# Performance work log

Hardware: AMD Instinct MI355X
Metric: run time of the kernel (lower is better)

## Reference

```python
import jax, jax.numpy as jnp
import numpy as np

N_NODES = 50000
N_EDGES = 1600000
D_IN = 256
N_HEADS = 4
D_OUT = 32
NEG_SLOPE = 0.2


def setup_inputs() -> dict:
    key = jax.random.key(0)
    ks = jax.random.split(key, 7)
    return {
        "feat": jax.random.normal(ks[0], (N_NODES, D_IN), dtype=jnp.float32),
        "fc_w": jax.random.normal(ks[1], (N_HEADS * D_OUT, D_IN), dtype=jnp.float32) * 0.05,
        "attn_l": jax.random.normal(ks[2], (1, N_HEADS, D_OUT), dtype=jnp.float32) * 0.1,
        "attn_r": jax.random.normal(ks[3], (1, N_HEADS, D_OUT), dtype=jnp.float32) * 0.1,
        "bias": jax.random.normal(ks[4], (N_HEADS * D_OUT,), dtype=jnp.float32) * 0.01,
        "src": jax.random.randint(ks[5], (N_EDGES,), 0, N_NODES, dtype=jnp.int32),
        "dst": jax.random.randint(ks[6], (N_EDGES,), 0, N_NODES, dtype=jnp.int32),
    }


def reference(feat, fc_w, attn_l, attn_r, bias, src, dst):
    N = feat.shape[0]
    H, D = attn_l.shape[1], attn_l.shape[2]
    # projected features: [N, H, D] (torch Linear: x @ W.T)
    h = (feat @ fc_w.T).reshape(N, H, D)
    # per-node attention logits: [N, H]
    el = (h * attn_l).sum(-1)
    er = (h * attn_r).sum(-1)
    # per-edge score with leaky relu: [E, H]
    e = el[src] + er[dst]
    e = jnp.where(e > 0, e, NEG_SLOPE * e)
    # edge softmax normalized over incoming edges of each dst node
    m = jax.ops.segment_max(e, dst, num_segments=N)
    m = jnp.where(jnp.isfinite(m), m, 0.0)  # nodes with no in-edges
    ex = jnp.exp(e - m[dst])
    denom = jax.ops.segment_sum(ex, dst, num_segments=N)
    a = ex / jnp.maximum(denom[dst], 1e-9)  # [E, H]
    # weighted scatter-aggregate: [N, H, D]
    msg = h[src] * a[:, :, None]
    out = jax.ops.segment_sum(msg, dst, num_segments=N)
    out = out + bias.reshape(1, H, D)
    return out
```

## Files before the change

### kernel.cpp

```cpp
#include <hip/hip_runtime.h>
#include <hip/hip_bf16.h>
#include <math.h>

#define D_IN   256
#define HD     128
#define NHEAD  4
#define NEG_SLOPE 0.2f
#define MAXB  1024
#define BCAP  2560

typedef _Float16 h8 __attribute__((ext_vector_type(8)));
typedef _Float16 h4 __attribute__((ext_vector_type(4)));
typedef _Float16 h2 __attribute__((ext_vector_type(2)));
typedef float f4 __attribute__((ext_vector_type(4)));

#define SWZ(row, byte) ((byte) ^ (((row) & 7) << 4))

__global__ __launch_bounds__(256) void fused_k(
        const float* __restrict__ feat, const float* __restrict__ fcw,
        const float* __restrict__ attn_l, const float* __restrict__ attn_r,
        unsigned int* __restrict__ hbuf, float* __restrict__ el, float* __restrict__ er,
        const int* __restrict__ src, const int* __restrict__ dst,
        int* __restrict__ gcur, unsigned int* __restrict__ pairs,
        int N, int E, int B, int GB) {
    __shared__ __align__(16) unsigned char smem[64 * 512];
    const int t = threadIdx.x;

    if ((int)blockIdx.x >= GB) {
        int* lcnt  = (int*)smem;
        int* lbase = lcnt + MAXB;
        for (int i = t; i < B; i += 256) lcnt[i] = 0;
        __syncthreads();
        const int base = ((int)blockIdx.x - GB) * 4096;
        int sv[16], dv[16];
        #pragma unroll
        for (int k = 0; k < 16; ++k) {
            int idx = base + k * 256 + t;
            if (idx < E) {
                sv[k] = src[idx];
                dv[k] = dst[idx];
                atomicAdd(&lcnt[dv[k] >> 6], 1);
            } else dv[k] = -1;
        }
        __syncthreads();
        for (int i = t; i < B; i += 256) {
            int c = lcnt[i];
            lbase[i] = c ? atomicAdd(&gcur[i], c) : 0;
            lcnt[i] = 0;
        }
        __syncthreads();
        #pragma unroll
        for (int k = 0; k < 16; ++k) {
            if (dv[k] >= 0) {
                int b = dv[k] >> 6;
                int r = lbase[b] + atomicAdd(&lcnt[b], 1);
                if (r < BCAP)
                    pairs[(size_t)b * BCAP + r] = ((unsigned int)sv[k] << 6) | (unsigned int)(dv[k] & 63);
            }
        }
        return;
    }

    unsigned char* lds_raw = smem;
    const int l  = t & 63;
    const int w  = t >> 6;
    const int l4 = l >> 4;
    const int lm = l & 15;
    const int n0 = blockIdx.x * 64;

    h8 breg[2][8];
    #pragma unroll
    for (int jt = 0; jt < 2; ++jt) {
        const float* wrow = fcw + (size_t)(w * 32 + jt * 16 + lm) * D_IN;
        #pragma unroll
        for (int ks = 0; ks < 8; ++ks) {
            int k = ks * 32 + l4 * 8;
            float4 a = *(const float4*)&wrow[k];
            float4 b = *(const float4*)&wrow[k + 4];
            h8 p = {(_Float16)a.x, (_Float16)a.y, (_Float16)a.z, (_Float16)a.w,
                    (_Float16)b.x, (_Float16)b.y, (_Float16)b.z, (_Float16)b.w};
            breg[jt][ks] = p;
        }
    }

    #pragma unroll
    for (int i = 0; i < 16; ++i) {
        int idx = t + 256 * i;
        int row = idx >> 6, c4 = idx & 63;
        float4 v = make_float4(0.f, 0.f, 0.f, 0.f);
        if (n0 + row < N) v = *(const float4*)&feat[(size_t)(n0 + row) * D_IN + c4 * 4];
        h4 p = {(_Float16)v.x, (_Float16)v.y, (_Float16)v.z, (_Float16)v.w};
        *(h4*)(lds_raw + row * 512 + SWZ(row, c4 * 8)) = p;
    }
    __syncthreads();

    f4 acc[4][2] = {};
    #pragma unroll
    for (int ks = 0; ks < 8; ++ks) {
        #pragma unroll
        for (int mt = 0; mt < 4; ++mt) {
            int row = mt * 16 + lm;
            h8 af = *(const h8*)(lds_raw + row * 512 + SWZ(row, (ks * 32 + l4 * 8) * 2));
            acc[mt][0] = __builtin_amdgcn_mfma_f32_16x16x32_f16(af, breg[0][ks], acc[mt][0], 0, 0, 0);
            acc[mt][1] = __builtin_amdgcn_mfma_f32_16x16x32_f16(af, breg[1][ks], acc[mt][1], 0, 0, 0);
        }
    }

    float al[2], ar[2];
    #pragma unroll
    for (int jt = 0; jt < 2; ++jt) {
        al[jt] = attn_l[w * 32 + jt * 16 + lm];
        ar[jt] = attn_r[w * 32 + jt * 16 + lm];
    }
    #pragma unroll
    for (int mt = 0; mt < 4; ++mt) {
        #pragma unroll
        for (int r = 0; r < 4; ++r) {
            float vl = acc[mt][0][r] * al[0] + acc[mt][1][r] * al[1];
            float vr = acc[mt][0][r] * ar[0] + acc[mt][1][r] * ar[1];
            #pragma unroll
            for (int o = 1; o < 16; o <<= 1) {
                vl += __shfl_xor(vl, o);
                vr += __shfl_xor(vr, o);
            }
            int node = n0 + mt * 16 + l4 * 4 + r;
            if (lm == 0 && node < N) {
                el[node * NHEAD + w] = vl;
                er[node * NHEAD + w] = vr;
            }
        }
    }

    __syncthreads();
    unsigned short* hl = (unsigned short*)lds_raw;
    #pragma unroll
    for (int mt = 0; mt < 4; ++mt)
        #pragma unroll
        for (int jt = 0; jt < 2; ++jt)
            #pragma unroll
            for (int r = 0; r < 4; ++r) {
                int node_local = mt * 16 + l4 * 4 + r;
                int ch = w * 32 + jt * 16 + lm;
                _Float16 hf = (_Float16)acc[mt][jt][r];
                hl[node_local * 128 + ch] = __builtin_bit_cast(unsigned short, hf);
            }
    __syncthreads();
    const unsigned int* hu = (const unsigned int*)lds_raw;
    #pragma unroll
    for (int i = 0; i < 16; ++i) {
        int idx = t + 256 * i;
        int row = idx >> 6, c = idx & 63;
        if (n0 + row < N) hbuf[(size_t)(n0 + row) * 64 + c] = hu[row * 64 + c];
    }
}

__global__ __launch_bounds__(256) void bucket_k(const unsigned int* __restrict__ pairs,
                                                const int* __restrict__ gcur,
                                                int* __restrict__ row_start,
                                                int* __restrict__ degs,
                                                int* __restrict__ srcs, int N) {
    __shared__ int cnt64[64];
    __shared__ int base64[64];
    const int b = blockIdx.x;
    const int t = threadIdx.x;
    const int lo = b * BCAP;
    const int len = min(gcur[b], BCAP);
    if (t < 64) cnt64[t] = 0;
    __syncthreads();
    for (int i = t; i < len; i += 256)
        atomicAdd(&cnt64[pairs[lo + i] & 63], 1);
    __syncthreads();
    if (t < 64) {
        int v = cnt64[t];
        int x = v;
        #pragma unroll
        for (int o = 1; o < 64; o <<= 1) {
            int y = __shfl_up(x, o);
            if (t >= o) x += y;
        }
        int excl = lo + x - v;
        base64[t] = excl;
        int d = b * 64 + t;
        if (d < N) { row_start[d] = excl; degs[d] = v; }
        cnt64[t] = 0;
    }
    __syncthreads();
    for (int i = lo + t; i < lo + len; i += 256) {
        unsigned int p = pairs[i];
        int ld = p & 63;
        int r = atomicAdd(&cnt64[ld], 1);
        srcs[base64[ld] + r] = (int)(p >> 6);
    }
}

__global__ __launch_bounds__(256) void agg_k(
        const int* __restrict__ row_start, const int* __restrict__ degs,
        const int* __restrict__ srcs,
        const float* __restrict__ el, const float* __restrict__ er,
        const unsigned int* __restrict__ hbuf, const float* __restrict__ bias,
        float* __restrict__ out, int N) {
    const int l = threadIdx.x & 63;
    const int d = blockIdx.x * 4 + (threadIdx.x >> 6);
    if (d >= N) return;
    const int q  = l >> 4;
    const int es = l & 15;
    const int hc = es >> 2;
    const int base = row_start[d];
    const int deg  = degs[d];
    const float erd = er[d * NHEAD + q];

    float acc[8] = {0.f, 0.f, 0.f, 0.f, 0.f, 0.f, 0.f, 0.f};
    float den = 0.f;

    for (int c0 = 0; c0 < deg; c0 += 32) {
        const int clen = min(32, deg - c0);
        int s0 = 0, s1 = 0;
        float ex0 = 0.f, ex1 = 0.f;
        if (es < clen) {
            s0 = srcs[base + c0 + es];
            float v = el[s0 * NHEAD + q] + erd;
            v = v > 0.f ? v : NEG_SLOPE * v;
            ex0 = __expf(v);
            den += ex0;
        }
        if (es + 16 < clen) {
            s1 = srcs[base + c0 + es + 16];
            float v = el[s1 * NHEAD + q] + erd;
            v = v > 0.f ? v : NEG_SLOPE * v;
            ex1 = __expf(v);
            den += ex1;
        }
        for (int jj = 0; jj < clen; jj += 16) {
            uint4 hv[4];
            float exv[4];
            #pragma unroll
            for (int k = 0; k < 4; ++k) {
                int e4 = jj + k * 4 + q;
                int ls = e4 & 15;
                int sa = __shfl(s0, ls);
                int sb = __shfl(s1, ls);
                float ea = __shfl(ex0, hc * 16 + ls);
                float eb = __shfl(ex1, hc * 16 + ls);
                int s = (e4 < 16) ? sa : sb;
                exv[k] = (e4 < clen) ? ((e4 < 16) ? ea : eb) : 0.f;
                hv[k] = *(const uint4*)&hbuf[(size_t)s * 64 + es * 4];
            }
            #pragma unroll
            for (int k = 0; k < 4; ++k) {
                #pragma unroll
                for (int c = 0; c < 4; ++c) {
                    unsigned int u = (&hv[k].x)[c];
                    h2 p = __builtin_bit_cast(h2, u);
                    acc[2 * c]     += (float)p[0] * exv[k];
                    acc[2 * c + 1] += (float)p[1] * exv[k];
                }
            }
        }
    }

    #pragma unroll
    for (int c = 0; c < 8; ++c) {
        acc[c] += __shfl_xor(acc[c], 16);
        acc[c] += __shfl_xor(acc[c], 32);
    }
    #pragma unroll
    for (int o = 1; o < 16; o <<= 1) den += __shfl_xor(den, o);
    float denc = __shfl(den, hc << 4);

    if (q == 0) {
        float r = 1.0f / fmaxf(denc, 1e-9f);
        float4 b0 = *(const float4*)&bias[es * 8];
        float4 b1 = *(const float4*)&bias[es * 8 + 4];
        float4 o0 = make_float4(acc[0] * r + b0.x, acc[1] * r + b0.y,
                                acc[2] * r + b0.z, acc[3] * r + b0.w);
        float4 o1 = make_float4(acc[4] * r + b1.x, acc[5] * r + b1.y,
                                acc[6] * r + b1.z, acc[7] * r + b1.w);
        *(float4*)&out[(size_t)d * HD + es * 8]     = o0;
        *(float4*)&out[(size_t)d * HD + es * 8 + 4] = o1;
    }
}

extern "C" void kernel_launch(void* const* d_in, const int* in_sizes, int n_in,
                              void* d_out, int out_size, void* d_ws, size_t ws_size,
                              hipStream_t stream) {
    const float* feat   = (const float*)d_in[0];
    const float* fcw    = (const float*)d_in[1];
    const float* attn_l = (const float*)d_in[2];
    const float* attn_r = (const float*)d_in[3];
    const float* bias   = (const float*)d_in[4];
    const int*   src    = (const int*)d_in[5];
    const int*   dst    = (const int*)d_in[6];
    float* out = (float*)d_out;

    const int N = in_sizes[0] / D_IN;
    const int E = in_sizes[5];
    const int B = (N + 63) >> 6;

    unsigned int* hbuf = (unsigned int*)d_ws;
    float* el        = (float*)(hbuf + (size_t)N * 64);
    float* er        = el + (size_t)N * NHEAD;
    unsigned int* pairs = (unsigned int*)(er + (size_t)N * NHEAD);
    int*   srcs      = (int*)(pairs + (size_t)B * BCAP);
    int*   row_start = srcs + (size_t)B * BCAP;
    int*   degs      = row_start + N;
    int*   gcur      = degs + N;

    const int GB  = (N + 63) / 64;
    const int ebl = (E + 4095) / 4096;

    hipMemsetAsync(gcur, 0, (size_t)B * sizeof(int), stream);
    fused_k<<<GB + ebl, 256, 0, stream>>>(feat, fcw, attn_l, attn_r, hbuf, el, er,
                                          src, dst, gcur, pairs, N, E, B, GB);
    bucket_k<<<B, 256, 0, stream>>>(pairs, gcur, row_start, degs, srcs, N);
    agg_k<<<(N + 3) / 4, 256, 0, stream>>>(row_start, degs, srcs, el, er, hbuf, bias, out, N);
}
```

Measured before the change: 131.7 us.

## Tile edges by source range and aggregate multiple destinations per wave for L2 locality

Edges are bucketed by destination block and by source-node quarter (src>>14), so bucketing produces per-(dst-block, src-tile) segments. The aggregation kernel has each wave own up to nine destination nodes and sweep the source tiles in order. The goal is to keep the gathered hbuf rows within a smaller working set that fits in cache. The aggregation also drops the shuffle-based 4-edge interleave in favour of one 32-bit channel pair per lane with four edges unrolled, which removes cross-lane reductions. In exchange it adds more segments and a smaller per-segment capacity (edges beyond it are dropped), fewer waves in flight, and possible load imbalance across waves.

```diff
diff --git a/kernel.cpp b/kernel.cpp
--- a/kernel.cpp
+++ b/kernel.cpp
@@ -6,8 +6,10 @@
 #define HD     128
 #define NHEAD  4
 #define NEG_SLOPE 0.2f
-#define MAXB  1024
-#define BCAP  2560
+#define T      4
+#define MAXK   4096
+#define SEGCAP 1024
+#define KMAX   9
 
 typedef _Float16 h8 __attribute__((ext_vector_type(8)));
 typedef _Float16 h4 __attribute__((ext_vector_type(4)));
@@ -22,14 +24,14 @@
         unsigned int* __restrict__ hbuf, float* __restrict__ el, float* __restrict__ er,
         const int* __restrict__ src, const int* __restrict__ dst,
         int* __restrict__ gcur, unsigned int* __restrict__ pairs,
-        int N, int E, int B, int GB) {
+        int N, int E, int B4, int GB) {
     __shared__ __align__(16) unsigned char smem[64 * 512];
     const int t = threadIdx.x;
 
     if ((int)blockIdx.x >= GB) {
         int* lcnt  = (int*)smem;
-        int* lbase = lcnt + MAXB;
-        for (int i = t; i < B; i += 256) lcnt[i] = 0;
+        int* lbase = lcnt + MAXK;
+        for (int i = t; i < B4; i += 256) lcnt[i] = 0;
         __syncthreads();
         const int base = ((int)blockIdx.x - GB) * 4096;
         int sv[16], dv[16];
@@ -39,11 +41,11 @@
             if (idx < E) {
                 sv[k] = src[idx];
                 dv[k] = dst[idx];
-                atomicAdd(&lcnt[dv[k] >> 6], 1);
+                atomicAdd(&lcnt[(dv[k] >> 6) * T + (sv[k] >> 14)], 1);
             } else dv[k] = -1;
         }
         __syncthreads();
-        for (int i = t; i < B; i += 256) {
+        for (int i = t; i < B4; i += 256) {
             int c = lcnt[i];
             lbase[i] = c ? atomicAdd(&gcur[i], c) : 0;
             lcnt[i] = 0;
@@ -52,10 +54,11 @@
         #pragma unroll
         for (int k = 0; k < 16; ++k) {
             if (dv[k] >= 0) {
-                int b = dv[k] >> 6;
-                int r = lbase[b] + atomicAdd(&lcnt[b], 1);
-                if (r < BCAP)
-                    pairs[(size_t)b * BCAP + r] = ((unsigned int)sv[k] << 6) | (unsigned int)(dv[k] & 63);
+                int key = (dv[k] >> 6) * T + (sv[k] >> 14);
+                int r = lbase[key] + atomicAdd(&lcnt[key], 1);
+                if (r < SEGCAP)
+                    pairs[(size_t)key * SEGCAP + r] =
+                        ((unsigned int)sv[k] << 6) | (unsigned int)(dv[k] & 63);
             }
         }
         return;
@@ -156,15 +159,16 @@
 
 __global__ __launch_bounds__(256) void bucket_k(const unsigned int* __restrict__ pairs,
                                                 const int* __restrict__ gcur,
-                                                int* __restrict__ row_start,
-                                                int* __restrict__ degs,
+                                                int2* __restrict__ rs2,
                                                 int* __restrict__ srcs, int N) {
     __shared__ int cnt64[64];
     __shared__ int base64[64];
-    const int b = blockIdx.x;
+    const int key = blockIdx.x;
+    const int b   = key / T;
+    const int tl  = key - b * T;
     const int t = threadIdx.x;
-    const int lo = b * BCAP;
-    const int len = min(gcur[b], BCAP);
+    const int lo = key * SEGCAP;
+    const int len = min(gcur[key], SEGCAP);
     if (t < 64) cnt64[t] = 0;
     __syncthreads();
     for (int i = t; i < len; i += 256)
@@ -181,7 +185,7 @@
         int excl = lo + x - v;
         base64[t] = excl;
         int d = b * 64 + t;
-        if (d < N) { row_start[d] = excl; degs[d] = v; }
+        if (d < N) rs2[d * T + tl] = make_int2(excl, v);
         cnt64[t] = 0;
     }
     __syncthreads();
@@ -194,89 +198,74 @@
 }
 
 __global__ __launch_bounds__(256) void agg_k(
-        const int* __restrict__ row_start, const int* __restrict__ degs,
-        const int* __restrict__ srcs,
+        const int2* __restrict__ rs2, const int* __restrict__ srcs,
         const float* __restrict__ el, const float* __restrict__ er,
         const unsigned int* __restrict__ hbuf, const float* __restrict__ bias,
-        float* __restrict__ out, int N) {
-    const int l = threadIdx.x & 63;
-    const int d = blockIdx.x * 4 + (threadIdx.x >> 6);
-    if (d >= N) return;
-    const int q  = l >> 4;
-    const int es = l & 15;
-    const int hc = es >> 2;
-    const int base = row_start[d];
-    const int deg  = degs[d];
-    const float erd = er[d * NHEAD + q];
-
-    float acc[8] = {0.f, 0.f, 0.f, 0.f, 0.f, 0.f, 0.f, 0.f};
-    float den = 0.f;
-
-    for (int c0 = 0; c0 < deg; c0 += 32) {
-        const int clen = min(32, deg - c0);
-        int s0 = 0, s1 = 0;
-        float ex0 = 0.f, ex1 = 0.f;
-        if (es < clen) {
-            s0 = srcs[base + c0 + es];
-            float v = el[s0 * NHEAD + q] + erd;
-            v = v > 0.f ? v : NEG_SLOPE * v;
-            ex0 = __expf(v);
-            den += ex0;
-        }
-        if (es + 16 < clen) {
-            s1 = srcs[base + c0 + es + 16];
-            float v = el[s1 * NHEAD + q] + erd;
-            v = v > 0.f ? v : NEG_SLOPE * v;
-            ex1 = __expf(v);
-            den += ex1;
-        }
-        for (int jj = 0; jj < clen; jj += 16) {
-            uint4 hv[4];
-            float exv[4];
-            #pragma unroll
-            for (int k = 0; k < 4; ++k) {
-                int e4 = jj + k * 4 + q;
-                int ls = e4 & 15;
-                int sa = __shfl(s0, ls);
-                int sb = __shfl(s1, ls);
-                float ea = __shfl(ex0, hc * 16 + ls);
-                float eb = __shfl(ex1, hc * 16 + ls);
-                int s = (e4 < 16) ? sa : sb;
-                exv[k] = (e4 < clen) ? ((e4 < 16) ? ea : eb) : 0.f;
-                hv[k] = *(const uint4*)&hbuf[(size_t)s * 64 + es * 4];
-            }
-            #pragma unroll
-            for (int k = 0; k < 4; ++k) {
-                #pragma unroll
-                for (int c = 0; c < 4; ++c) {
-                    unsigned int u = (&hv[k].x)[c];
-                    h2 p = __builtin_bit_cast(h2, u);
-                    acc[2 * c]     += (float)p[0] * exv[k];
-                    acc[2 * c + 1] += (float)p[1] * exv[k];
+        float* __restrict__ out, int N, int stride) {
+    const int l  = threadIdx.x & 63;
+    const int g  = blockIdx.x * 4 + (threadIdx.x >> 6);
+    const int h  = l >> 4;
+
+    float ax[KMAX], ay[KMAX], dn[KMAX];
+    #pragma unroll
+    for (int k = 0; k < KMAX; ++k) { ax[k] = 0.f; ay[k] = 0.f; dn[k] = 0.f; }
+
+    for (int tl = 0; tl < T; ++tl) {
+        #pragma unroll
+        for (int k = 0; k < KMAX; ++k) {
+            const int d = g + k * stride;
+            if (d < N) {
+                const int2 bd = rs2[d * T + tl];
+                const int deg = bd.y;
+                if (deg > 0) {
+                    const float erd = er[d * NHEAD + h];
+                    for (int j = 0; j < deg; j += 4) {
+                        const int n = deg - j;
+                        const int jb = bd.x + j;
+                        int s0 = srcs[jb];
+                        int s1 = (n > 1) ? srcs[jb + 1] : 0;
+                        int s2 = (n > 2) ? srcs[jb + 2] : 0;
+                        int s3 = (n > 3) ? srcs[jb + 3] : 0;
+                        float e0 = el[s0 * NHEAD + h];
+                        float e1 = el[s1 * NHEAD + h];
+                        float e2 = el[s2 * NHEAD + h];
+                        float e3 = el[s3 * NHEAD + h];
+                        unsigned int v0 = hbuf[(size_t)s0 * 64 + l];
+                        unsigned int v1 = hbuf[(size_t)s1 * 64 + l];
+                        unsigned int v2 = hbuf[(size_t)s2 * 64 + l];
+                        unsigned int v3 = hbuf[(size_t)s3 * 64 + l];
+                        float q0 = e0 + erd; q0 = q0 > 0.f ? q0 : NEG_SLOPE * q0;
+                        float q1 = e1 + erd; q1 = q1 > 0.f ? q1 : NEG_SLOPE * q1;
+                        float q2 = e2 + erd; q2 = q2 > 0.f ? q2 : NEG_SLOPE * q2;
+                        float q3 = e3 + erd; q3 = q3 > 0.f ? q3 : NEG_SLOPE * q3;
+                        float x0 = __expf(q0);
+                        float x1 = (n > 1) ? __expf(q1) : 0.f;
+                        float x2 = (n > 2) ? __expf(q2) : 0.f;
+                        float x3 = (n > 3) ? __expf(q3) : 0.f;
+                        dn[k] += (x0 + x1) + (x2 + x3);
+                        h2 p0 = __builtin_bit_cast(h2, v0);
+                        h2 p1 = __builtin_bit_cast(h2, v1);
+                        h2 p2 = __builtin_bit_cast(h2, v2);
+                        h2 p3 = __builtin_bit_cast(h2, v3);
+                        ax[k] += (float)p0[0] * x0 + (float)p1[0] * x1
+                               + (float)p2[0] * x2 + (float)p3[0] * x3;
+                        ay[k] += (float)p0[1] * x0 + (float)p1[1] * x1
+                               + (float)p2[1] * x2 + (float)p3[1] * x3;
+                    }
                 }
             }
         }
     }
 
-    #pragma unroll
-    for (int c = 0; c < 8; ++c) {
-        acc[c] += __shfl_xor(acc[c], 16);
-        acc[c] += __shfl_xor(acc[c], 32);
-    }
-    #pragma unroll
-    for (int o = 1; o < 16; o <<= 1) den += __shfl_xor(den, o);
-    float denc = __shfl(den, hc << 4);
-
-    if (q == 0) {
-        float r = 1.0f / fmaxf(denc, 1e-9f);
-        float4 b0 = *(const float4*)&bias[es * 8];
-        float4 b1 = *(const float4*)&bias[es * 8 + 4];
-        float4 o0 = make_float4(acc[0] * r + b0.x, acc[1] * r + b0.y,
-                                acc[2] * r + b0.z, acc[3] * r + b0.w);
-        float4 o1 = make_float4(acc[4] * r + b1.x, acc[5] * r + b1.y,
-                                acc[6] * r + b1.z, acc[7] * r + b1.w);
-        *(float4*)&out[(size_t)d * HD + es * 8]     = o0;
-        *(float4*)&out[(size_t)d * HD + es * 8 + 4] = o1;
+    const float2 bb = *(const float2*)&bias[2 * l];
+    #pragma unroll
+    for (int k = 0; k < KMAX; ++k) {
+        const int d = g + k * stride;
+        if (d < N) {
+            float r = 1.0f / fmaxf(dn[k], 1e-9f);
+            float2 o2 = make_float2(ax[k] * r + bb.x, ay[k] * r + bb.y);
+            *(float2*)&out[(size_t)d * HD + 2 * l] = o2;
+        }
     }
 }
 
@@ -295,22 +284,25 @@
     const int N = in_sizes[0] / D_IN;
     const int E = in_sizes[5];
     const int B = (N + 63) >> 6;
+    const int B4 = B * T;
 
     unsigned int* hbuf = (unsigned int*)d_ws;
     float* el        = (float*)(hbuf + (size_t)N * 64);
     float* er        = el + (size_t)N * NHEAD;
     unsigned int* pairs = (unsigned int*)(er + (size_t)N * NHEAD);
-    int*   srcs      = (int*)(pairs + (size_t)B * BCAP);
-    int*   row_start = srcs + (size_t)B * BCAP;
-    int*   degs      = row_start + N;
-    int*   gcur      = degs + N;
+    int*   srcs      = (int*)(pairs + (size_t)B4 * SEGCAP);
+    int2*  rs2       = (int2*)(srcs + (size_t)B4 * SEGCAP);
+    int*   gcur      = (int*)(rs2 + (size_t)N * T);
 
     const int GB  = (N + 63) / 64;
     const int ebl = (E + 4095) / 4096;
 
-    hipMemsetAsync(gcur, 0, (size_t)B * sizeof(int), stream);
+    const int aggBlocks = (N + 4 * KMAX - 1) / (4 * KMAX);
+    const int stride = aggBlocks * 4;
+
+    hipMemsetAsync(gcur, 0, (size_t)B4 * sizeof(int), stream);
     fused_k<<<GB + ebl, 256, 0, stream>>>(feat, fcw, attn_l, attn_r, hbuf, el, er,
-                                          src, dst, gcur, pairs, N, E, B, GB);
-    bucket_k<<<B, 256, 0, stream>>>(pairs, gcur, row_start, degs, srcs, N);
-    agg_k<<<(N + 3) / 4, 256, 0, stream>>>(row_start, degs, srcs, el, er, hbuf, bias, out, N);
+                                          src, dst, gcur, pairs, N, E, B4, GB);
+    bucket_k<<<B4, 256, 0, stream>>>(pairs, gcur, rs2, srcs, N);
+    agg_k<<<aggBlocks, 256, 0, stream>>>(rs2, srcs, el, er, hbuf, bias, out, N, stride);
 }
```

After: 229.0 us (median of 4 runs). 73.9% more time.
